# Kernel tuning notes

Hardware: AMD Instinct MI355X
Metric: run time of the kernel (lower is better)

## Reference

```python
import jax, jax.numpy as jnp
import numpy as np

BOUND = 2.3  # default non-learnable bound


def setup_inputs() -> dict:
    key = jax.random.key(0)
    k1, k2, k3, k4 = jax.random.split(key, 4)
    B, C, H, W = 64, 256, 56, 56
    n_points = 7  # n_regions=6
    x = jax.random.normal(k1, (B, C, H, W), dtype=jnp.float32)
    # learned per-channel breakpoint values (relu-like init would be monotone;
    # random values are fine for a correctness baseline)
    points = jax.random.normal(k2, (C, n_points), dtype=jnp.float32)
    left_diffs = jax.random.normal(k3, (C,), dtype=jnp.float32)
    right_diffs = jax.random.normal(k4, (C,), dtype=jnp.float32)
    return {"x": x, "points": points, "left_diffs": left_diffs, "right_diffs": right_diffs}


def reference(x, points, left_diffs, right_diffs):
    # channelwise PWLU, scalar (non-learnable) bounds
    n_points = points.shape[-1]
    n_regions = n_points - 1
    left_b, right_b = -BOUND, BOUND
    region_len = (right_b - left_b) / n_regions          # scalar
    sim_left = left_b - region_len                        # extra region left of bound

    x_normal = (x - sim_left) / region_len                # [B,C,H,W]
    regions = jnp.clip(x_normal, 0.0, (n_regions + 1) * 1.001).astype(jnp.int32)
    dists = x_normal - regions.astype(x.dtype)

    # per-region slopes table: [C, n_points+1]
    diffs = jnp.concatenate(
        [left_diffs[:, None], points[..., 1:] - points[..., :-1], right_diffs[:, None]],
        axis=-1,
    )
    # points table extended with the effective point left of the left bound: [C, n_points+1]
    false_points = jnp.concatenate([(points[..., 0] - left_diffs)[:, None], points], axis=-1)

    C = points.shape[0]
    ch = jnp.arange(C)[None, :, None, None]               # broadcast channel index
    left_points = false_points[ch, regions]               # gather [B,C,H,W]
    slopes = diffs[ch, regions]
    return left_points + dists * slopes
```

## Files before the change

### kernel.cpp

```cpp
#include <hip/hip_runtime.h>


constexpr int NP   = 7;
constexpr int NT   = 8;
constexpr int CH   = 256;
constexpr int HW   = 56 * 56;
constexpr int HW4  = HW / 4;
constexpr int PPB  = 16;
constexpr int F4PB = PPB * HW4;
constexpr int UN   = 7;

typedef float f4 __attribute__((ext_vector_type(4)));

__device__ __forceinline__ float pwlu1(float xv, const float2* __restrict__ tc) {
    constexpr float sim_left = -3.0666666666666664f;
    constexpr float inv_len  = 1.3043478260869565f;
    constexpr float hi       = 7.007f;
    const float xn = (xv - sim_left) * inv_len;
    const int   r  = (int)fminf(fmaxf(xn, 0.0f), hi);
    const float2 t = tc[r];
    return fmaf(xn - (float)r, t.y, t.x);
}

__device__ __forceinline__ f4 pwlu4(f4 v, const float2* __restrict__ tc) {
    f4 o;
    o.x = pwlu1(v.x, tc);
    o.y = pwlu1(v.y, tc);
    o.z = pwlu1(v.z, tc);
    o.w = pwlu1(v.w, tc);
    return o;
}

template<int IT>
__device__ __forceinline__ void load7(f4* v, const f4* __restrict__ xp) {
#pragma unroll
    for (int j = 0; j < UN; ++j)
        v[j] = __builtin_nontemporal_load(xp + (IT * UN + j) * 256);
}

template<int IT>
__device__ __forceinline__ void proc7(const f4* v, f4* __restrict__ op,
                                      const float2* __restrict__ tbl,
                                      int cbase, int tid) {
#pragma unroll
    for (int j = 0; j < UN; ++j) {
        const int idx = IT * UN + j;
        const int pl  = (int)((unsigned)(idx * 256 + tid) / 784u);
        const float2* tc = tbl + ((cbase + pl) << 3);
        __builtin_nontemporal_store(pwlu4(v[j], tc), op + idx * 256);
    }
}

__global__ __launch_bounds__(256, 4) void pwlu_kernel(
    const f4* __restrict__ x,
    const float* __restrict__ points,
    const float* __restrict__ left_diffs,
    const float* __restrict__ right_diffs,
    f4* __restrict__ out)
{
    __shared__ float2 tbl[CH * NT];

    const int tid = threadIdx.x;
    const size_t base = (size_t)blockIdx.x * F4PB;
    const f4* __restrict__ xp = x + base + tid;
    f4*       __restrict__ op = out + base + tid;

    f4 va[UN], vb[UN];
    load7<0>(va, xp);

    {
        const int r  = tid & 7;
        const int c0 = tid >> 3;
#pragma unroll
        for (int k = 0; k < NT; ++k) {
            const int c = k * 32 + c0;
            const float* p = points + c * NP;
            float fp, df;
            if (r == 0)       { const float ld = left_diffs[c]; fp = p[0] - ld;  df = ld; }
            else if (r == NP) { fp = p[NP - 1];                  df = right_diffs[c]; }
            else              { const float a = p[r - 1], b = p[r]; fp = a; df = b - a; }
            tbl[c * NT + r] = make_float2(fp, df);
        }
    }
    __syncthreads();

    const int cbase = (blockIdx.x & (CH / PPB - 1)) * PPB;

    load7<1>(vb, xp); proc7<0>(va, op, tbl, cbase, tid);
    load7<2>(va, xp); proc7<1>(vb, op, tbl, cbase, tid);
    load7<3>(vb, xp); proc7<2>(va, op, tbl, cbase, tid);
    load7<4>(va, xp); proc7<3>(vb, op, tbl, cbase, tid);
    load7<5>(vb, xp); proc7<4>(va, op, tbl, cbase, tid);
    load7<6>(va, xp); proc7<5>(vb, op, tbl, cbase, tid);
    proc7<6>(va, op, tbl, cbase, tid);
}

extern "C" void kernel_launch(void* const* d_in, const int* in_sizes, int n_in,
                              void* d_out, int out_size, void* d_ws, size_t ws_size,
                              hipStream_t stream) {
    const f4*    x  = (const f4*)d_in[0];
    const float* pt = (const float*)d_in[1];
    const float* ld = (const float*)d_in[2];
    const float* rd = (const float*)d_in[3];
    f4*          o  = (f4*)d_out;

    const int planes = in_sizes[0] / HW;
    pwlu_kernel<<<planes / PPB, 256, 0, stream>>>(x, pt, ld, rd, o);
}
```

Baseline: 343.2 us.

## Use many small blocks with a per-block local channel table

Replaces the 16-plane-per-block kernel, which built a full 256-channel table and ran a software-pipelined 49-iteration loop, with small blocks that each process 8 float4 per thread. Each block now builds only the table rows for the at most 4 planes it touches. This cuts per-block table setup and exposes far more blocks for latency hiding and load balance, at the cost of more block launches and a sync in every short block. It also drops the explicit load/compute double-buffering and the launch_bounds occupancy hint.

```diff
diff --git a/kernel.cpp b/kernel.cpp
--- a/kernel.cpp
+++ b/kernel.cpp
@@ -2,13 +2,10 @@
 
 
 constexpr int NP   = 7;
-constexpr int NT   = 8;
-constexpr int CH   = 256;
 constexpr int HW   = 56 * 56;
 constexpr int HW4  = HW / 4;
-constexpr int PPB  = 16;
-constexpr int F4PB = PPB * HW4;
-constexpr int UN   = 7;
+constexpr int K    = 8;
+constexpr int F4PB = 256 * K;
 
 typedef float f4 __attribute__((ext_vector_type(4)));
 
@@ -31,68 +28,47 @@
     return o;
 }
 
-template<int IT>
-__device__ __forceinline__ void load7(f4* v, const f4* __restrict__ xp) {
-#pragma unroll
-    for (int j = 0; j < UN; ++j)
-        v[j] = __builtin_nontemporal_load(xp + (IT * UN + j) * 256);
-}
-
-template<int IT>
-__device__ __forceinline__ void proc7(const f4* v, f4* __restrict__ op,
-                                      const float2* __restrict__ tbl,
-                                      int cbase, int tid) {
-#pragma unroll
-    for (int j = 0; j < UN; ++j) {
-        const int idx = IT * UN + j;
-        const int pl  = (int)((unsigned)(idx * 256 + tid) / 784u);
-        const float2* tc = tbl + ((cbase + pl) << 3);
-        __builtin_nontemporal_store(pwlu4(v[j], tc), op + idx * 256);
-    }
-}
-
-__global__ __launch_bounds__(256, 4) void pwlu_kernel(
+__global__ __launch_bounds__(256) void pwlu_kernel(
     const f4* __restrict__ x,
     const float* __restrict__ points,
     const float* __restrict__ left_diffs,
     const float* __restrict__ right_diffs,
     f4* __restrict__ out)
 {
-    __shared__ float2 tbl[CH * NT];
+    __shared__ float2 tbl[4 * 8];
 
     const int tid = threadIdx.x;
-    const size_t base = (size_t)blockIdx.x * F4PB;
+    const unsigned base = (unsigned)blockIdx.x * F4PB;
+
     const f4* __restrict__ xp = x + base + tid;
-    f4*       __restrict__ op = out + base + tid;
+    f4 v[K];
+#pragma unroll
+    for (int j = 0; j < K; ++j)
+        v[j] = __builtin_nontemporal_load(xp + j * 256);
 
-    f4 va[UN], vb[UN];
-    load7<0>(va, xp);
+    const unsigned plane_lo = base / 784u;
 
-    {
-        const int r  = tid & 7;
-        const int c0 = tid >> 3;
-#pragma unroll
-        for (int k = 0; k < NT; ++k) {
-            const int c = k * 32 + c0;
-            const float* p = points + c * NP;
-            float fp, df;
-            if (r == 0)       { const float ld = left_diffs[c]; fp = p[0] - ld;  df = ld; }
-            else if (r == NP) { fp = p[NP - 1];                  df = right_diffs[c]; }
-            else              { const float a = p[r - 1], b = p[r]; fp = a; df = b - a; }
-            tbl[c * NT + r] = make_float2(fp, df);
-        }
+    if (tid < 32) {
+        const int rel = tid >> 3;
+        const int r   = tid & 7;
+        const int c   = (int)((plane_lo + rel) & 255u);
+        const float* p = points + c * NP;
+        float fp, df;
+        if (r == 0)       { const float ld = left_diffs[c]; fp = p[0] - ld;  df = ld; }
+        else if (r == NP) { fp = p[NP - 1];                  df = right_diffs[c]; }
+        else              { const float a = p[r - 1], b = p[r]; fp = a; df = b - a; }
+        tbl[tid] = make_float2(fp, df);
     }
     __syncthreads();
 
-    const int cbase = (blockIdx.x & (CH / PPB - 1)) * PPB;
-
-    load7<1>(vb, xp); proc7<0>(va, op, tbl, cbase, tid);
-    load7<2>(va, xp); proc7<1>(vb, op, tbl, cbase, tid);
-    load7<3>(vb, xp); proc7<2>(va, op, tbl, cbase, tid);
-    load7<4>(va, xp); proc7<3>(vb, op, tbl, cbase, tid);
-    load7<5>(vb, xp); proc7<4>(va, op, tbl, cbase, tid);
-    load7<6>(va, xp); proc7<5>(vb, op, tbl, cbase, tid);
-    proc7<6>(va, op, tbl, cbase, tid);
+    f4* __restrict__ op = out + base + tid;
+#pragma unroll
+    for (int j = 0; j < K; ++j) {
+        const unsigned idx = base + j * 256u + (unsigned)tid;
+        const int rel = (int)(idx / 784u - plane_lo);
+        const float2* tc = tbl + (rel << 3);
+        __builtin_nontemporal_store(pwlu4(v[j], tc), op + j * 256);
+    }
 }
 
 extern "C" void kernel_launch(void* const* d_in, const int* in_sizes, int n_in,
@@ -105,5 +81,6 @@
     f4*          o  = (f4*)d_out;
 
     const int planes = in_sizes[0] / HW;
-    pwlu_kernel<<<planes / PPB, 256, 0, stream>>>(x, pt, ld, rd, o);
+    const int blocks = planes * HW4 / F4PB;
+    pwlu_kernel<<<blocks, 256, 0, stream>>>(x, pt, ld, rd, o);
 }
```

Result: faster. 327.8 us (-4.5%).
